# Kernel tuning notes

Hardware: AMD Instinct MI355X
Metric: run time of the kernel (lower is better)

The kernel has to match this reference:

```python
import jax, jax.numpy as jnp
import numpy as np
from itertools import combinations

A = 4          # anchor_points
K = 16         # neighbor_num
INTRA = A * (A - 1) // 2   # 6
CH = INTRA * 2 + A * A     # 28 = generator channels
B, N, S = 1, 8192, 4096
CIN, COUT = 64, 128


def cdist(x):
    # pairwise euclidean distances [B,N,N], zero-safe sqrt (zero grad at d=0)
    sq = jnp.sum(x * x, -1)
    d2 = sq[:, :, None] + sq[:, None, :] - 2.0 * jnp.einsum('bnc,bmc->bnm', x, x)
    d2 = jnp.maximum(d2, 0.0)
    m = d2 > 0
    return jnp.where(m, jnp.sqrt(jnp.where(m, d2, 1.0)), 0.0)


def index_points(points, idx):
    # points [B,N,...], idx [B,*] -> [B,*,...]
    return jax.vmap(lambda p, i: p[i])(points, idx)


def index_points_dists(dists, i1, i2):
    # dists [B,N,N]; result[b,...] = dists[b, i1[b,...], i2[b,...]]
    i1, i2 = jnp.broadcast_arrays(i1, i2)
    return jax.vmap(lambda d, a, b: d[a, b])(dists, i1, i2)


def generator(xyz):
    # RotationInvariantDistFea.forward(xyz, concat_raw_relative_fea=True)
    D = cdist(xyz)
    neg_nd, ni = jax.lax.top_k(-D, K)   # K >= A; smallest-K, sorted ascending
    nd = -neg_nd
    ai = ni[:, :, :A]
    # intra-anchor dists: dists to anchors 1..A-1 plus pairwise dists among them
    subs = [index_points_dists(D, ai[:, :, pi], ai[:, :, pj])[:, :, None]
            for pi, pj in combinations(range(1, A), 2)]
    intra = jnp.concatenate([nd[:, :, 1:A]] + subs, axis=2)  # [B,P,6]
    # inter-anchor dists: center anchors x neighbor anchors -> [B,P,K,A*A]
    nai = index_points(ai, ni)                                # [B,P,K,A]
    inter = index_points_dists(D, ai[:, :, None, :, None],
                               nai[:, :, :, None, :]).reshape(D.shape[0], D.shape[1], K, A * A)
    center = jnp.broadcast_to(intra[:, :, None, :], (intra.shape[0], intra.shape[1], K, INTRA))
    rf = jnp.concatenate([center, index_points(intra, ni), inter], axis=3)  # [B,P,K,28]
    return rf, ni, D


def mlp(x, W, b, g, be, act):
    # Linear + BatchNorm1d (training mode: stats over batch*points) + optional leaky_relu(0.2)
    y = x @ W + b
    mu = jnp.mean(y, (0, 1))
    var = jnp.var(y, (0, 1))
    y = (y - mu) * jax.lax.rsqrt(var + 1e-5) * g + be
    return jax.nn.leaky_relu(y, 0.2) if act else y


def forward(xyz, feature, sample_indexes, Ww, bw, gw, betaw, Wb, bb, gb, betab, Wo, bo, go, betao):
    rf_before, ni_before, D_before = generator(xyz)
    intra_before = rf_before[:, :, 0, :INTRA]
    xyz_s = index_points(xyz, sample_indexes)
    feat = index_points(feature, sample_indexes)
    intra_before = index_points(intra_before, sample_indexes)
    rf_after, ni_after, _ = generator(xyz_s)
    intra_after = rf_after[:, :, 0, :INTRA]
    a_before = index_points(ni_before[:, :, :A], sample_indexes)                  # [B,S,A]
    a_after = jax.vmap(lambda s, a: s[a])(sample_indexes, ni_after[:, :, :A])     # map to global idx
    inter = index_points_dists(D_before, a_before[:, :, :, None],
                               a_after[:, :, None, :]).reshape(B, S, A * A)
    adf = jnp.concatenate([intra_before, intra_after, inter], axis=2)             # [B,S,28]
    w = mlp(adf, Ww, bw, gw, betaw, False)
    bia = mlp(adf, Wb, bb, gb, betab, False)
    feat = jax.nn.leaky_relu(feat * w + bia, 0.2)
    feat = jnp.concatenate([feat, adf], axis=2)                                   # [B,S,92]
    feat = mlp(feat, Wo, bo, go, betao, True)                                     # [B,S,128]
    return xyz_s, feat, rf_after, ni_after


def setup_inputs():
    key = jax.random.key(0)
    ks = jax.random.split(key, 8)
    xyz = jax.random.normal(ks[0], (B, N, 3), jnp.float32)
    feature = jax.random.normal(ks[1], (B, N, CIN), jnp.float32)
    sample_indexes = jnp.stack([jax.random.permutation(jax.random.fold_in(ks[2], i), N)[:S]
                                for i in range(B)]).astype(jnp.int32)

    def lin(k, cin, cout):
        k1, k2 = jax.random.split(k)
        W = jax.random.normal(k1, (cin, cout), jnp.float32) / np.float32(np.sqrt(cin))
        b = jax.random.normal(k2, (cout,), jnp.float32) * 0.01
        return W, b, jnp.ones((cout,), jnp.float32), jnp.zeros((cout,), jnp.float32)

    Ww, bw, gw, betaw = lin(ks[5], CH, CIN)
    Wb, bb, gb, betab = lin(ks[6], CH, CIN)
    Wo, bo, go, betao = lin(ks[7], CH + CIN, COUT)
    return dict(xyz=xyz, feature=feature, sample_indexes=sample_indexes,
                Ww=Ww, bw=bw, gw=gw, betaw=betaw,
                Wb=Wb, bb=bb, gb=gb, betab=betab,
                Wo=Wo, bo=bo, go=go, betao=betao)


def reference(xyz, feature, sample_indexes, Ww, bw, gw, betaw, Wb, bb, gb, betab, Wo, bo, go, betao):
    return forward(xyz, feature, sample_indexes, Ww, bw, gw, betaw, Wb, bb, gb, betab, Wo, bo, go, betao)
```

## Files before the change

### kernel.cpp

```cpp
#include <hip/hip_runtime.h>
#include <hip/hip_bf16.h>
#include <math.h>

#define N_PTS 8192
#define S_PTS 4096
typedef unsigned long long u64;
typedef unsigned u32;

__device__ __forceinline__ float pair_dist_d(const float4 a, const float4 b) {
    double ax = a.x, ay = a.y, az = a.z;
    double bx = b.x, by = b.y, bz = b.z;
    double dx = ax - bx, dy = ay - by, dz = az - bz;
    double d2 = dx * dx + dy * dy + dz * dz;
    return d2 > 0.0 ? (float)sqrt(d2) : 0.0f;
}

__device__ __forceinline__ float d2_f32_gram(const float4 a, const float4 b) {
    float dot = __fadd_rn(__fadd_rn(__fmul_rn(a.x, b.x), __fmul_rn(a.y, b.y)),
                          __fmul_rn(a.z, b.z));
    float d2 = __fsub_rn(__fadd_rn(a.w, b.w), __fmul_rn(2.0f, dot));
    return fmaxf(d2, 0.0f);
}

__global__ __launch_bounds__(256) void stage_kernel(
        const float* __restrict__ xyz, const int* __restrict__ sidx,
        float4* __restrict__ cb, float4* __restrict__ ca,
        float* __restrict__ out_xyz_s) {
    int i = blockIdx.x * blockDim.x + threadIdx.x;
    if (i < N_PTS) {
        float x = xyz[i * 3 + 0], y = xyz[i * 3 + 1], z = xyz[i * 3 + 2];
        float sq = __fadd_rn(__fadd_rn(__fmul_rn(x, x), __fmul_rn(y, y)),
                             __fmul_rn(z, z));
        cb[i] = make_float4(x, y, z, sq);
    }
    if (i < S_PTS) {
        int si = sidx[i];
        float x = xyz[si * 3 + 0], y = xyz[si * 3 + 1], z = xyz[si * 3 + 2];
        float sq = __fadd_rn(__fadd_rn(__fmul_rn(x, x), __fmul_rn(y, y)),
                             __fmul_rn(z, z));
        ca[i] = make_float4(x, y, z, sq);
        out_xyz_s[i * 3 + 0] = x;
        out_xyz_s[i * 3 + 1] = y;
        out_xyz_s[i * 3 + 2] = z;
    }
}


template <int KOUT, int ITERS>
__device__ u64 knn_full_ladder(const float4 q, const float4* __restrict__ cand,
                               int lane) {
    u32 Lk[KOUT], Li[KOUT];
#pragma unroll
    for (int j = 0; j < KOUT; ++j) { Lk[j] = 0xFFFFFFFFu; Li[j] = 0xFFFFFFFFu; }
    int c = lane;
    for (int tt = 0; tt < ITERS; ++tt, c += 64) {
        float d2 = d2_f32_gram(q, cand[c]);
        float Df = d2 > 0.0f ? __fsqrt_rn(d2) : 0.0f;
        u32 kb = __float_as_uint(Df);
        if (kb < Lk[KOUT - 1]) {
#pragma unroll
            for (int j = KOUT - 1; j >= 1; --j) {
                bool up = kb < Lk[j - 1], ins = kb < Lk[j];
                Lk[j] = up ? Lk[j - 1] : (ins ? kb : Lk[j]);
                Li[j] = up ? Li[j - 1] : (ins ? (u32)c : Li[j]);
            }
            bool i0 = kb < Lk[0];
            Lk[0] = i0 ? kb : Lk[0];
            Li[0] = i0 ? (u32)c : Li[0];
        }
    }
    u64 Lu[KOUT];
#pragma unroll
    for (int j = 0; j < KOUT; ++j) Lu[j] = ((u64)Lk[j] << 32) | (u64)Li[j];
    u64 res = ~0ull;
#pragma unroll
    for (int r = 0; r < KOUT; ++r) {
        u64 m = Lu[0];
#pragma unroll
        for (int off = 32; off >= 1; off >>= 1) {
            u64 o = __shfl_xor(m, off, 64);
            m = (o < m) ? o : m;
        }
        if (lane == r) res = m;
        if (Lu[0] == m) {
#pragma unroll
            for (int j = 0; j < KOUT - 1; ++j) Lu[j] = Lu[j + 1];
            Lu[KOUT - 1] = ~0ull;
        }
    }
    return res;
}

template <int J, int K, int NC>
__device__ u64 knn_select(const float4 q, const float4* __restrict__ cand,
                          int t, u32* mins, u64* buf, u32* shm) {
    int lane = t & 63, wid = t >> 6;
    u32 d2b[J];
    u32 m = 0xFFFFFFFFu;
#pragma unroll
    for (int j = 0; j < J; ++j) {
        float d2 = d2_f32_gram(q, cand[t + 256 * j]);
        u32 b = __float_as_uint(d2);
        d2b[j] = b;
        m = b < m ? b : m;
    }
    mins[t] = m;
    __syncthreads();
    if (wid == 0) {
        u32 v = mins[lane];
        u32 v2 = mins[lane + 64];  v = v2 < v ? v2 : v;
        v2 = mins[lane + 128];     v = v2 < v ? v2 : v;
        v2 = mins[lane + 192];     v = v2 < v ? v2 : v;
#pragma unroll
        for (int k = 2; k <= 64; k <<= 1) {
#pragma unroll
            for (int j2 = k >> 1; j2 >= 1; j2 >>= 1) {
                u32 o = __shfl_xor(v, j2, 64);
                bool keepMin = (((lane & j2) == 0) == ((lane & k) == 0));
                bool less = o < v;
                v = keepMin ? (less ? o : v) : (less ? v : o);
            }
        }
        if (lane == K - 1) shm[0] = v;
    }
    __syncthreads();
    u32 tau = shm[0];
    u32 c = 0;
#pragma unroll
    for (int j = 0; j < J; ++j) c += (d2b[j] <= tau) ? 1u : 0u;
    u32 x = c;
#pragma unroll
    for (int off = 1; off < 64; off <<= 1) {
        u32 y = __shfl_up(x, off, 64);
        if (lane >= off) x += y;
    }
    if (lane == 63) shm[1 + wid] = x;
    __syncthreads();
    u32 base = x - c;
    for (int w = 0; w < wid; ++w) base += shm[1 + w];
    u32 cnt = shm[1] + shm[2] + shm[3] + shm[4];
    if (cnt <= 256u) {
        u32 off = base;
#pragma unroll
        for (int j = 0; j < J; ++j) {
            if (d2b[j] <= tau) {
                float d2 = __uint_as_float(d2b[j]);
                float D = d2 > 0.0f ? __fsqrt_rn(d2) : 0.0f;
                buf[off++] = ((u64)__float_as_uint(D) << 32) |
                             (u64)(u32)(t + 256 * j);
            }
        }
    }
    __syncthreads();
    u64 res = ~0ull;
    if (wid == 0) {
        if (cnt <= 64u) {
            u64 v = (lane < (int)cnt) ? buf[lane] : ~0ull;
#pragma unroll
            for (int k = 2; k <= 64; k <<= 1) {
#pragma unroll
                for (int j2 = k >> 1; j2 >= 1; j2 >>= 1) {
                    u64 o = __shfl_xor(v, j2, 64);
                    bool keepMin = (((lane & j2) == 0) == ((lane & k) == 0));
                    bool less = o < v;
                    v = keepMin ? (less ? o : v) : (less ? v : o);
                }
            }
            res = v;
        } else if (cnt <= 256u) {
            u64 L0 = ~0ull, L1 = ~0ull, L2 = ~0ull, L3 = ~0ull;
            for (u32 mm = lane; mm < cnt; mm += 64) {
                u64 kk = buf[mm];
                if (kk < L3) {
                    if (kk < L1) {
                        L3 = L2; L2 = L1;
                        if (kk < L0) { L1 = L0; L0 = kk; } else L1 = kk;
                    } else {
                        if (kk < L2) { L3 = L2; L2 = kk; } else L3 = kk;
                    }
                }
            }
#pragma unroll
            for (int r = 0; r < K; ++r) {
                u64 mr = L0;
#pragma unroll
                for (int off = 32; off >= 1; off >>= 1) {
                    u64 o = __shfl_xor(mr, off, 64);
                    mr = (o < mr) ? o : mr;
                }
                if (lane == r) res = mr;
                if (L0 == mr) { L0 = L1; L1 = L2; L2 = L3; L3 = ~0ull; }
            }
        } else {
            res = knn_full_ladder<K, NC / 64>(q, cand, lane);
        }
    }
    return res;
}

__global__ __launch_bounds__(256, 4) void knn_kernel(
        const float4* __restrict__ cb, const float4* __restrict__ ca,
        const int* __restrict__ sidx,
        int* __restrict__ a_before, float* __restrict__ intra_before,
        int* __restrict__ ni_i, float* __restrict__ intra_after,
        float* __restrict__ out_ni) {
    __shared__ u32 mins[256];
    __shared__ u64 buf[256];
    __shared__ u32 shm[8];
    int t = threadIdx.x, lane = t & 63, wid = t >> 6;
    int bid = blockIdx.x;
    if (bid < S_PTS) {
        int s = bid;
        float4 q = ca[s];
        u64 res = knn_select<16, 16, 4096>(q, ca, t, mins, buf, shm);
        if (wid == 0) {
            int idx = (int)(res & 0xffffffffull);
            if (lane < 16) {
                ni_i[s * 16 + lane] = idx;
                out_ni[s * 16 + lane] = (float)idx;
            }
            if (lane >= 1 && lane < 4)
                intra_after[s * 6 + (lane - 1)] = pair_dist_d(q, ca[idx]);
            int i1 = __shfl(idx, 1, 64);
            int i2 = __shfl(idx, 2, 64);
            int i3 = __shfl(idx, 3, 64);
            if (lane < 3) {
                int pa = (lane == 2) ? i2 : i1;
                int pb = (lane == 0) ? i2 : i3;
                intra_after[s * 6 + 3 + lane] = pair_dist_d(ca[pa], ca[pb]);
            }
        }
    } else {
        int s = bid - S_PTS;
        float4 q = cb[sidx[s]];
        u64 res = knn_select<32, 4, 8192>(q, cb, t, mins, buf, shm);
        if (wid == 0) {
            int idx = (int)(res & 0xffffffffull);
            if (lane < 4) a_before[s * 4 + lane] = idx;
            if (lane >= 1 && lane < 4)
                intra_before[s * 6 + (lane - 1)] = pair_dist_d(q, cb[idx]);
            int i1 = __shfl(idx, 1, 64);
            int i2 = __shfl(idx, 2, 64);
            int i3 = __shfl(idx, 3, 64);
            if (lane < 3) {
                int pa = (lane == 2) ? i2 : i1;
                int pb = (lane == 0) ? i2 : i3;
                intra_before[s * 6 + 3 + lane] = pair_dist_d(cb[pa], cb[pb]);
            }
        }
    }
}

__global__ __launch_bounds__(256) void assemble_kernel(
        const float4* __restrict__ ca, const float4* __restrict__ cb,
        const int* __restrict__ ni_i, const float* __restrict__ intra_after,
        const int* __restrict__ a_before, const float* __restrict__ intra_before,
        const int* __restrict__ sidx,
        float* __restrict__ out_rf, float* __restrict__ adf) {
    __shared__ int s_ni[4][16];
    __shared__ float s_rf[4][16 * 28];
    __shared__ float s_ia[4][8];
    int t = threadIdx.x, wid = t >> 6, lane = t & 63;
    int s = blockIdx.x * 4 + wid;
    if (lane < 16) s_ni[wid][lane] = ni_i[s * 16 + lane];
    if (lane < 6) s_ia[wid][lane] = intra_after[s * 6 + lane];
    __syncthreads();

    int k = lane >> 2, qq = lane & 3;
    int nai_q = ni_i[s_ni[wid][k] * 16 + qq];
    float4 pq = ca[nai_q];
#pragma unroll
    for (int p = 0; p < 4; ++p) {
        float4 pp = ca[s_ni[wid][p]];
        s_rf[wid][k * 28 + 12 + p * 4 + qq] = pair_dist_d(pp, pq);
    }
    for (int idx = lane; idx < 16 * 12; idx += 64) {
        int kk = idx / 12, c = idx % 12;
        float v = (c < 6) ? s_ia[wid][c] : intra_after[s_ni[wid][kk] * 6 + (c - 6)];
        s_rf[wid][kk * 28 + c] = v;
    }
    if (lane < 16) {
        int p = lane >> 2, q2 = lane & 3;
        int ib = a_before[s * 4 + p];
        int ia = sidx[s_ni[wid][q2]];
        adf[s * 28 + 12 + lane] = pair_dist_d(cb[ib], cb[ia]);
    } else if (lane >= 32 && lane < 38) {
        adf[s * 28 + (lane - 32)] = intra_before[s * 6 + (lane - 32)];
    } else if (lane >= 40 && lane < 46) {
        adf[s * 28 + 6 + (lane - 40)] = s_ia[wid][lane - 40];
    }
    __syncthreads();
    const int base = s * 16 * 28;
    for (int idx = lane; idx < 16 * 28; idx += 64) out_rf[base + idx] = s_rf[wid][idx];
}

__global__ __launch_bounds__(256) void mlp1_kernel(
        const float* __restrict__ adf,
        const float* __restrict__ Ww, const float* __restrict__ bw,
        const float* __restrict__ Wb, const float* __restrict__ bb,
        float* __restrict__ y_wb) {
    __shared__ float sW[28 * 128];
    __shared__ float sb[128];
    __shared__ float sA[32 * 28];
    int t = threadIdx.x;
    for (int i = t; i < 28 * 128; i += 256) {
        int k = i >> 7, c = i & 127;
        sW[i] = (c < 64) ? Ww[k * 64 + c] : Wb[k * 64 + (c - 64)];
    }
    if (t < 128) sb[t] = (t < 64) ? bw[t] : bb[t - 64];
    int s0 = blockIdx.x * 32;
    for (int i = t; i < 32 * 28; i += 256) sA[i] = adf[s0 * 28 + i];
    __syncthreads();
    int sl = t >> 3, grp = t & 7;
    int s = s0 + sl;
    float acc[16];
#pragma unroll
    for (int k = 0; k < 16; ++k) acc[k] = sb[grp * 16 + k];
    for (int k2 = 0; k2 < 28; ++k2) {
        float a = sA[sl * 28 + k2];
#pragma unroll
        for (int k = 0; k < 16; ++k)
            acc[k] = fmaf(a, sW[k2 * 128 + grp * 16 + k], acc[k]);
    }
#pragma unroll
    for (int k = 0; k < 16; ++k) y_wb[(grp * 16 + k) * 4096 + s] = acc[k];
}

__global__ __launch_bounds__(256) void stats_kernel(
        const float* __restrict__ y,
        const float* __restrict__ g0, const float* __restrict__ be0,
        const float* __restrict__ g1, const float* __restrict__ be1, int csplit,
        float* __restrict__ scale, float* __restrict__ shift) {
    int c = blockIdx.x;
    const float* p = y + c * 4096;
    float s1 = 0.0f, s2 = 0.0f;
    for (int i = threadIdx.x; i < 4096; i += 256) {
        float v = p[i];
        s1 += v;
        s2 = fmaf(v, v, s2);
    }
    __shared__ float l1[256], l2[256];
    l1[threadIdx.x] = s1;
    l2[threadIdx.x] = s2;
    __syncthreads();
    for (int off = 128; off; off >>= 1) {
        if (threadIdx.x < off) {
            l1[threadIdx.x] += l1[threadIdx.x + off];
            l2[threadIdx.x] += l2[threadIdx.x + off];
        }
        __syncthreads();
    }
    if (threadIdx.x == 0) {
        float mean = l1[0] * (1.0f / 4096.0f);
        float var = l2[0] * (1.0f / 4096.0f) - mean * mean;
        float g = (c < csplit) ? g0[c] : g1[c - csplit];
        float be = (c < csplit) ? be0[c] : be1[c - csplit];
        float sc = g / sqrtf(var + 1e-5f);
        scale[c] = sc;
        shift[c] = be - mean * sc;
    }
}

__global__ __launch_bounds__(256) void mlp2_kernel(
        const float* __restrict__ y_wb,
        const float* __restrict__ scale1, const float* __restrict__ shift1,
        const float* __restrict__ feature, const int* __restrict__ sidx,
        const float* __restrict__ adf,
        const float* __restrict__ Wo, const float* __restrict__ bo,
        float* __restrict__ y_o) {
    __shared__ float sW[92 * 128];
    __shared__ float t2[16 * 129];
    __shared__ float scat[16 * 92];
    int t = threadIdx.x;
    int s0 = blockIdx.x * 16;
    for (int i = t; i < 92 * 128; i += 256) sW[i] = Wo[i];
    for (int i = t; i < 16 * 128; i += 256) {
        int row = i & 15, c = i >> 4;
        t2[row * 129 + c] = fmaf(y_wb[c * 4096 + s0 + row], scale1[c], shift1[c]);
    }
    __syncthreads();
    for (int rr = 0; rr < 16; rr += 4) {
        int r = rr + (t >> 6);
        int c = t & 63;
        int si = sidx[s0 + r];
        float f = feature[si * 64 + c];
        float v = fmaf(f, t2[r * 129 + c], t2[r * 129 + 64 + c]);
        scat[r * 92 + c] = v >= 0.0f ? v : 0.2f * v;
    }
    for (int i = t; i < 16 * 28; i += 256) {
        int row = i / 28, k = i % 28;
        scat[row * 92 + 64 + k] = adf[(s0 + row) * 28 + k];
    }
    __syncthreads();
    int r = t >> 4, cg = t & 15;
    float acc[8];
#pragma unroll
    for (int j = 0; j < 8; ++j) acc[j] = bo[cg * 8 + j];
    for (int c = 0; c < 92; ++c) {
        float a = scat[r * 92 + c];
#pragma unroll
        for (int j = 0; j < 8; ++j)
            acc[j] = fmaf(a, sW[c * 128 + cg * 8 + j], acc[j]);
    }
    int s = s0 + r;
#pragma unroll
    for (int j = 0; j < 8; ++j) y_o[(cg * 8 + j) * 4096 + s] = acc[j];
}

__global__ __launch_bounds__(256) void final_kernel(
        const float* __restrict__ y_o,
        const float* __restrict__ scale, const float* __restrict__ shift,
        float* __restrict__ out_feat) {
    int tid = blockIdx.x * 256 + threadIdx.x;
    int j = tid >> 12;
    int s = tid & 4095;
    float v = fmaf(y_o[tid], scale[j], shift[j]);
    v = v >= 0.0f ? v : 0.2f * v;
    out_feat[s * 128 + j] = v;
}

extern "C" void kernel_launch(void* const* d_in, const int* in_sizes, int n_in,
                              void* d_out, int out_size, void* d_ws, size_t ws_size,
                              hipStream_t stream) {
    const float* xyz = (const float*)d_in[0];
    const float* feature = (const float*)d_in[1];
    const int* sidx = (const int*)d_in[2];
    const float* Ww = (const float*)d_in[3];
    const float* bw = (const float*)d_in[4];
    const float* gw = (const float*)d_in[5];
    const float* betaw = (const float*)d_in[6];
    const float* Wb = (const float*)d_in[7];
    const float* bb = (const float*)d_in[8];
    const float* gb = (const float*)d_in[9];
    const float* betab = (const float*)d_in[10];
    const float* Wo = (const float*)d_in[11];
    const float* bo = (const float*)d_in[12];
    const float* go = (const float*)d_in[13];
    const float* betao = (const float*)d_in[14];

    float* out = (float*)d_out;
    float* out_xyz = out;
    float* out_feat = out + 12288;
    float* out_rf = out + 12288 + 524288;
    float* out_ni = out + 12288 + 524288 + 1835008;

    float* ws = (float*)d_ws;
    float4* cb = (float4*)ws;
    float4* ca = (float4*)(ws + 32768);
    int* a_before = (int*)(ws + 49152);
    float* intra_before = ws + 65536;
    int* ni_i = (int*)(ws + 90112);
    float* intra_after = ws + 155648;
    float* adf = ws + 180224;
    float* y_wb = ws + 294912;
    float* y_o = ws + 819200;
    float* scale1 = ws + 1343488;
    float* shift1 = ws + 1343616;
    float* scale_o = ws + 1343744;
    float* shift_o = ws + 1343872;

    stage_kernel<<<32, 256, 0, stream>>>(xyz, sidx, cb, ca, out_xyz);
    knn_kernel<<<2 * S_PTS, 256, 0, stream>>>(cb, ca, sidx, a_before, intra_before,
                                              ni_i, intra_after, out_ni);
    assemble_kernel<<<1024, 256, 0, stream>>>(ca, cb, ni_i, intra_after, a_before,
                                              intra_before, sidx, out_rf, adf);
    mlp1_kernel<<<128, 256, 0, stream>>>(adf, Ww, bw, Wb, bb, y_wb);
    stats_kernel<<<128, 256, 0, stream>>>(y_wb, gw, betaw, gb, betab, 64, scale1, shift1);
    mlp2_kernel<<<256, 256, 0, stream>>>(y_wb, scale1, shift1, feature, sidx, adf, Wo, bo, y_o);
    stats_kernel<<<128, 256, 0, stream>>>(y_o, go, betao, go, betao, 128, scale_o, shift_o);
    final_kernel<<<2048, 256, 0, stream>>>(y_o, scale_o, shift_o, out_feat);
}
```

Before: 171.8 us.

## Batch multiple KNN queries per block to reuse candidate loads

Each KNN block now handles 4 queries for the 'after' set and 2 for the 'before' set. Every candidate point is loaded once and compared against all queries in the block, and the selection work is split across waves, one wave per query. This cuts the redundant global reads of candidates and the per-block sync overhead. In exchange it raises register pressure (d2b grows to Q×J), uses more shared memory, and launches fewer blocks, which can lower occupancy under launch_bounds(256,4).

```diff
diff --git a/kernel.cpp b/kernel.cpp
--- a/kernel.cpp
+++ b/kernel.cpp
@@ -91,26 +91,80 @@
     return res;
 }
 
-template <int J, int K, int NC>
-__device__ u64 knn_select(const float4 q, const float4* __restrict__ cand,
-                          int t, u32* mins, u64* buf, u32* shm) {
+template <int K, int NC>
+__device__ u64 final_select(const float4 qq, const float4* __restrict__ cand,
+                            const u64* bufq, u32 cnt, int lane) {
+    if (cnt <= 64u) {
+        u64 v = (lane < (int)cnt) ? bufq[lane] : ~0ull;
+#pragma unroll
+        for (int k = 2; k <= 64; k <<= 1) {
+#pragma unroll
+            for (int j2 = k >> 1; j2 >= 1; j2 >>= 1) {
+                u64 o = __shfl_xor(v, j2, 64);
+                bool keepMin = (((lane & j2) == 0) == ((lane & k) == 0));
+                bool less = o < v;
+                v = keepMin ? (less ? o : v) : (less ? v : o);
+            }
+        }
+        return v;
+    } else if (cnt <= 256u) {
+        u64 L0 = ~0ull, L1 = ~0ull, L2 = ~0ull, L3 = ~0ull;
+        for (u32 mm = lane; mm < cnt; mm += 64) {
+            u64 kk = bufq[mm];
+            if (kk < L3) {
+                if (kk < L1) {
+                    L3 = L2; L2 = L1;
+                    if (kk < L0) { L1 = L0; L0 = kk; } else L1 = kk;
+                } else {
+                    if (kk < L2) { L3 = L2; L2 = kk; } else L3 = kk;
+                }
+            }
+        }
+        u64 res = ~0ull;
+#pragma unroll
+        for (int r = 0; r < K; ++r) {
+            u64 mr = L0;
+#pragma unroll
+            for (int off = 32; off >= 1; off >>= 1) {
+                u64 o = __shfl_xor(mr, off, 64);
+                mr = (o < mr) ? o : mr;
+            }
+            if (lane == r) res = mr;
+            if (L0 == mr) { L0 = L1; L1 = L2; L2 = L3; L3 = ~0ull; }
+        }
+        return res;
+    }
+    return knn_full_ladder<K, NC / 64>(qq, cand, lane);
+}
+
+template <int J, int K, int NC, int Q>
+__device__ __forceinline__ u64 knn_selectq(
+        const float4* qs, const float4* __restrict__ cand, int t,
+        u32* mins, u64* buf, u32* shm) {
     int lane = t & 63, wid = t >> 6;
-    u32 d2b[J];
-    u32 m = 0xFFFFFFFFu;
+    u32 d2b[Q][J];
+    u32 m[Q];
+#pragma unroll
+    for (int qi = 0; qi < Q; ++qi) m[qi] = 0xFFFFFFFFu;
 #pragma unroll
     for (int j = 0; j < J; ++j) {
-        float d2 = d2_f32_gram(q, cand[t + 256 * j]);
-        u32 b = __float_as_uint(d2);
-        d2b[j] = b;
-        m = b < m ? b : m;
-    }
-    mins[t] = m;
-    __syncthreads();
-    if (wid == 0) {
-        u32 v = mins[lane];
-        u32 v2 = mins[lane + 64];  v = v2 < v ? v2 : v;
-        v2 = mins[lane + 128];     v = v2 < v ? v2 : v;
-        v2 = mins[lane + 192];     v = v2 < v ? v2 : v;
+        float4 c = cand[t + 256 * j];
+#pragma unroll
+        for (int qi = 0; qi < Q; ++qi) {
+            u32 b = __float_as_uint(d2_f32_gram(qs[qi], c));
+            d2b[qi][j] = b;
+            m[qi] = b < m[qi] ? b : m[qi];
+        }
+    }
+#pragma unroll
+    for (int qi = 0; qi < Q; ++qi) mins[qi * 256 + t] = m[qi];
+    __syncthreads();
+    if (wid < Q) {
+        const u32* mq = mins + wid * 256;
+        u32 v = mq[lane];
+        u32 v2 = mq[lane + 64];  v = v2 < v ? v2 : v;
+        v2 = mq[lane + 128];     v = v2 < v ? v2 : v;
+        v2 = mq[lane + 192];     v = v2 < v ? v2 : v;
 #pragma unroll
         for (int k = 2; k <= 64; k <<= 1) {
 #pragma unroll
@@ -121,80 +175,53 @@
                 v = keepMin ? (less ? o : v) : (less ? v : o);
             }
         }
-        if (lane == K - 1) shm[0] = v;
-    }
-    __syncthreads();
-    u32 tau = shm[0];
-    u32 c = 0;
-#pragma unroll
-    for (int j = 0; j < J; ++j) c += (d2b[j] <= tau) ? 1u : 0u;
-    u32 x = c;
-#pragma unroll
-    for (int off = 1; off < 64; off <<= 1) {
-        u32 y = __shfl_up(x, off, 64);
-        if (lane >= off) x += y;
-    }
-    if (lane == 63) shm[1 + wid] = x;
-    __syncthreads();
-    u32 base = x - c;
-    for (int w = 0; w < wid; ++w) base += shm[1 + w];
-    u32 cnt = shm[1] + shm[2] + shm[3] + shm[4];
-    if (cnt <= 256u) {
-        u32 off = base;
-#pragma unroll
-        for (int j = 0; j < J; ++j) {
-            if (d2b[j] <= tau) {
-                float d2 = __uint_as_float(d2b[j]);
-                float D = d2 > 0.0f ? __fsqrt_rn(d2) : 0.0f;
-                buf[off++] = ((u64)__float_as_uint(D) << 32) |
-                             (u64)(u32)(t + 256 * j);
+        if (lane == K - 1) shm[wid] = v;
+    }
+    __syncthreads();
+    u32 tau[Q], c[Q], x[Q];
+#pragma unroll
+    for (int qi = 0; qi < Q; ++qi) {
+        tau[qi] = shm[qi];
+        u32 cc = 0;
+#pragma unroll
+        for (int j = 0; j < J; ++j) cc += (d2b[qi][j] <= tau[qi]) ? 1u : 0u;
+        c[qi] = cc;
+        u32 xx = cc;
+#pragma unroll
+        for (int off = 1; off < 64; off <<= 1) {
+            u32 y = __shfl_up(xx, off, 64);
+            if (lane >= off) xx += y;
+        }
+        x[qi] = xx;
+        if (lane == 63) shm[Q + qi * 4 + wid] = xx;
+    }
+    __syncthreads();
+    u32 cnt[Q];
+#pragma unroll
+    for (int qi = 0; qi < Q; ++qi) {
+        u32 base = x[qi] - c[qi];
+        for (int w = 0; w < wid; ++w) base += shm[Q + qi * 4 + w];
+        cnt[qi] = shm[Q + qi * 4 + 0] + shm[Q + qi * 4 + 1] +
+                  shm[Q + qi * 4 + 2] + shm[Q + qi * 4 + 3];
+        if (cnt[qi] <= 256u) {
+            u32 off = base;
+#pragma unroll
+            for (int j = 0; j < J; ++j) {
+                if (d2b[qi][j] <= tau[qi]) {
+                    float d2 = __uint_as_float(d2b[qi][j]);
+                    float D = d2 > 0.0f ? __fsqrt_rn(d2) : 0.0f;
+                    buf[qi * 256 + off++] = ((u64)__float_as_uint(D) << 32) |
+                                            (u64)(u32)(t + 256 * j);
+                }
             }
         }
     }
     __syncthreads();
     u64 res = ~0ull;
-    if (wid == 0) {
-        if (cnt <= 64u) {
-            u64 v = (lane < (int)cnt) ? buf[lane] : ~0ull;
-#pragma unroll
-            for (int k = 2; k <= 64; k <<= 1) {
-#pragma unroll
-                for (int j2 = k >> 1; j2 >= 1; j2 >>= 1) {
-                    u64 o = __shfl_xor(v, j2, 64);
-                    bool keepMin = (((lane & j2) == 0) == ((lane & k) == 0));
-                    bool less = o < v;
-                    v = keepMin ? (less ? o : v) : (less ? v : o);
-                }
-            }
-            res = v;
-        } else if (cnt <= 256u) {
-            u64 L0 = ~0ull, L1 = ~0ull, L2 = ~0ull, L3 = ~0ull;
-            for (u32 mm = lane; mm < cnt; mm += 64) {
-                u64 kk = buf[mm];
-                if (kk < L3) {
-                    if (kk < L1) {
-                        L3 = L2; L2 = L1;
-                        if (kk < L0) { L1 = L0; L0 = kk; } else L1 = kk;
-                    } else {
-                        if (kk < L2) { L3 = L2; L2 = kk; } else L3 = kk;
-                    }
-                }
-            }
-#pragma unroll
-            for (int r = 0; r < K; ++r) {
-                u64 mr = L0;
-#pragma unroll
-                for (int off = 32; off >= 1; off >>= 1) {
-                    u64 o = __shfl_xor(mr, off, 64);
-                    mr = (o < mr) ? o : mr;
-                }
-                if (lane == r) res = mr;
-                if (L0 == mr) { L0 = L1; L1 = L2; L2 = L3; L3 = ~0ull; }
-            }
-        } else {
-            res = knn_full_ladder<K, NC / 64>(q, cand, lane);
-        }
-    }
+#pragma unroll
+    for (int qi = 0; qi < Q; ++qi)
+        if (wid == qi)
+            res = final_select<K, NC>(qs[qi], cand, buf + qi * 256, cnt[qi], lane);
     return res;
 }
 
@@ -204,23 +231,27 @@
         int* __restrict__ a_before, float* __restrict__ intra_before,
         int* __restrict__ ni_i, float* __restrict__ intra_after,
         float* __restrict__ out_ni) {
-    __shared__ u32 mins[256];
-    __shared__ u64 buf[256];
-    __shared__ u32 shm[8];
+    __shared__ u32 mins[4 * 256];
+    __shared__ u64 buf[4 * 256];
+    __shared__ u32 shm[24];
     int t = threadIdx.x, lane = t & 63, wid = t >> 6;
     int bid = blockIdx.x;
-    if (bid < S_PTS) {
-        int s = bid;
-        float4 q = ca[s];
-        u64 res = knn_select<16, 16, 4096>(q, ca, t, mins, buf, shm);
-        if (wid == 0) {
+    if (bid < S_PTS / 4) {
+        int s0 = bid * 4;
+        float4 qs[4];
+#pragma unroll
+        for (int qi = 0; qi < 4; ++qi) qs[qi] = ca[s0 + qi];
+        u64 res = knn_selectq<16, 16, 4096, 4>(qs, ca, t, mins, buf, shm);
+        if (wid < 4) {
+            int s = s0 + wid;
+            float4 qq = ca[s];
             int idx = (int)(res & 0xffffffffull);
             if (lane < 16) {
                 ni_i[s * 16 + lane] = idx;
                 out_ni[s * 16 + lane] = (float)idx;
             }
             if (lane >= 1 && lane < 4)
-                intra_after[s * 6 + (lane - 1)] = pair_dist_d(q, ca[idx]);
+                intra_after[s * 6 + (lane - 1)] = pair_dist_d(qq, ca[idx]);
             int i1 = __shfl(idx, 1, 64);
             int i2 = __shfl(idx, 2, 64);
             int i3 = __shfl(idx, 3, 64);
@@ -231,14 +262,18 @@
             }
         }
     } else {
-        int s = bid - S_PTS;
-        float4 q = cb[sidx[s]];
-        u64 res = knn_select<32, 4, 8192>(q, cb, t, mins, buf, shm);
-        if (wid == 0) {
+        int s0 = (bid - S_PTS / 4) * 2;
+        float4 qs[2];
+        qs[0] = cb[sidx[s0]];
+        qs[1] = cb[sidx[s0 + 1]];
+        u64 res = knn_selectq<32, 4, 8192, 2>(qs, cb, t, mins, buf, shm);
+        if (wid < 2) {
+            int s = s0 + wid;
+            float4 qq = cb[sidx[s]];
             int idx = (int)(res & 0xffffffffull);
             if (lane < 4) a_before[s * 4 + lane] = idx;
             if (lane >= 1 && lane < 4)
-                intra_before[s * 6 + (lane - 1)] = pair_dist_d(q, cb[idx]);
+                intra_before[s * 6 + (lane - 1)] = pair_dist_d(qq, cb[idx]);
             int i1 = __shfl(idx, 1, 64);
             int i2 = __shfl(idx, 2, 64);
             int i3 = __shfl(idx, 3, 64);
@@ -460,8 +495,8 @@
     float* shift_o = ws + 1343872;
 
     stage_kernel<<<32, 256, 0, stream>>>(xyz, sidx, cb, ca, out_xyz);
-    knn_kernel<<<2 * S_PTS, 256, 0, stream>>>(cb, ca, sidx, a_before, intra_before,
-                                              ni_i, intra_after, out_ni);
+    knn_kernel<<<S_PTS / 4 + S_PTS / 2, 256, 0, stream>>>(
+        cb, ca, sidx, a_before, intra_before, ni_i, intra_after, out_ni);
     assemble_kernel<<<1024, 256, 0, stream>>>(ca, cb, ni_i, intra_after, a_before,
                                               intra_before, sidx, out_rf, adf);
     mlp1_kernel<<<128, 256, 0, stream>>>(adf, Ww, bw, Wb, bb, y_wb);
```

New measurement: 166.6 us. 1.03x faster.
